# Kernel tuning notes

Hardware: AMD Instinct MI355X
Metric: run time of the kernel (lower is better)

The kernel has to match this reference:

```python
import jax, jax.numpy as jnp
import numpy as np

D_MODEL = 1024
NUM_HEAD = 16
D_HEAD = 64


def setup_inputs() -> dict:
    key = jax.random.key(0)
    ks = jax.random.split(key, 9)
    b, p = 8, 1024
    s = 1.0 / np.sqrt(D_MODEL)
    inp = {
        "x": jax.random.normal(ks[0], (b, p, D_MODEL), jnp.float32),
        "w_q": jax.random.uniform(ks[1], (D_MODEL, D_MODEL), jnp.float32, -s, s),
        "b_q": jax.random.uniform(ks[2], (D_MODEL,), jnp.float32, -s, s),
        "w_k": jax.random.uniform(ks[3], (D_MODEL, D_MODEL), jnp.float32, -s, s),
        "b_k": jax.random.uniform(ks[4], (D_MODEL,), jnp.float32, -s, s),
        "w_v": jax.random.uniform(ks[5], (D_MODEL, D_MODEL), jnp.float32, -s, s),
        "b_v": jax.random.uniform(ks[6], (D_MODEL,), jnp.float32, -s, s),
        "w_o": jax.random.uniform(ks[7], (D_MODEL, D_MODEL), jnp.float32, -s, s),
        "b_o": jax.random.uniform(ks[8], (D_MODEL,), jnp.float32, -s, s),
    }
    return inp


def reference(x, w_q, b_q, w_k, b_k, w_v, b_v, w_o, b_o):
    b, p, _ = x.shape
    # projections (torch Linear: y = x @ W.T + b; here weights stored [in,out])
    q = x @ w_q + b_q
    k = x @ w_k + b_k
    v = x @ w_v + b_v
    # [b, h, p, d]
    q = q.reshape(b, p, NUM_HEAD, D_HEAD).transpose(0, 2, 1, 3)
    k = k.reshape(b, p, NUM_HEAD, D_HEAD).transpose(0, 2, 1, 3)
    v = v.reshape(b, p, NUM_HEAD, D_HEAD).transpose(0, 2, 1, 3)
    scale = 1.0 / np.sqrt(D_HEAD).astype(np.float32)
    scores = jnp.einsum("bhqd,bhkd->bhqk", q, k) * scale
    attn = jax.nn.softmax(scores, axis=-1)
    out = jnp.einsum("bhqk,bhkd->bhqd", attn, v)
    out = out.transpose(0, 2, 1, 3).reshape(b, p, D_MODEL)
    return out @ w_o + b_o
```

## Files before the change

kernel.cpp:

```cpp
#include <hip/hip_runtime.h>
#include <stdint.h>


typedef __attribute__((ext_vector_type(8))) short short8;
typedef __attribute__((ext_vector_type(4))) short s16x4;
typedef __attribute__((ext_vector_type(4))) float f32x4;

__device__ __forceinline__ short f2bf(float f) {
  unsigned u = __builtin_bit_cast(unsigned, f);
  u += 0x7fffu + ((u >> 16) & 1u);
  return (short)(u >> 16);
}

__device__ __forceinline__ unsigned pk2bf(float a, float b) {
  unsigned ua = __builtin_bit_cast(unsigned, a);
  unsigned ub = __builtin_bit_cast(unsigned, b);
  ua += 0x7fffu + ((ua >> 16) & 1u);
  ub += 0x7fffu + ((ub >> 16) & 1u);
  return (ua >> 16) | (ub & 0xffff0000u);
}

typedef __attribute__((address_space(3))) void lds_void;
typedef __attribute__((address_space(1))) void gbl_void;
#define GLD16(gp, lp) \
  __builtin_amdgcn_global_load_lds((gbl_void*)(gp), (lds_void*)(lp), 16, 0, 0)

#define MFMA(a, b, c) __builtin_amdgcn_mfma_f32_16x16x32_bf16((a), (b), (c), 0, 0, 0)

__global__ __launch_bounds__(256) void k_convert(const float* __restrict__ src,
                                                 short* __restrict__ dst) {
  int i = (blockIdx.x * 256 + threadIdx.x) * 8;
  const float4* s = (const float4*)(src + i);
  float4 f0 = s[0], f1 = s[1];
  short8 o;
  o[0] = f2bf(f0.x); o[1] = f2bf(f0.y); o[2] = f2bf(f0.z); o[3] = f2bf(f0.w);
  o[4] = f2bf(f1.x); o[5] = f2bf(f1.y); o[6] = f2bf(f1.z); o[7] = f2bf(f1.w);
  *(short8*)(dst + i) = o;
}

__global__ __launch_bounds__(256) void k_transpose4(const float* __restrict__ s0,
                                                    const float* __restrict__ s1,
                                                    const float* __restrict__ s2,
                                                    const float* __restrict__ s3,
                                                    short* __restrict__ d0,
                                                    short* __restrict__ d1,
                                                    short* __restrict__ d2,
                                                    short* __restrict__ d3) {
  __shared__ float tile[32][33];
  const float* srcs[4] = {s0, s1, s2, s3};
  short* dsts[4] = {d0, d1, d2, d3};
  const float* src = srcs[blockIdx.z];
  short* dst = dsts[blockIdx.z];
  int tx = threadIdx.x, ty = threadIdx.y;
  int x0 = blockIdx.x * 32, y0 = blockIdx.y * 32;
#pragma unroll
  for (int i = 0; i < 32; i += 8)
    tile[ty + i][tx] = src[(y0 + ty + i) * 1024 + x0 + tx];
  __syncthreads();
#pragma unroll
  for (int i = 0; i < 32; i += 8)
    dst[(x0 + ty + i) * 1024 + y0 + tx] = f2bf(tile[tx][ty + i]);
}

template <int MODE>
__global__ __launch_bounds__(256, 3) void k_gemm(const short* __restrict__ A,
                                                 const short* __restrict__ Bt,
                                                 const float* __restrict__ bias0,
                                                 const float* __restrict__ bias1,
                                                 const float* __restrict__ bias2,
                                                 short* __restrict__ o0,
                                                 short* __restrict__ o1,
                                                 short* __restrict__ o2,
                                                 float* __restrict__ of) {
  __shared__ __align__(16) short a_lds[128 * 64];
  __shared__ __align__(16) short b_lds[128 * 64];
  const int tid = threadIdx.x;
  const int m0 = blockIdx.y * 128;
  const int n0 = blockIdx.x * 128;
  const int w = tid >> 6;
  const int lane = tid & 63;
  const int ll = lane & 15;
  const int qd = lane >> 4;
  const int wm = (w & 1) * 64;
  const int wn = (w >> 1) * 64;

  const int srow = tid >> 3;
  const int schunk = ((tid & 7) ^ (srow & 7)) * 8;
  const short* ag = A + (long)(m0 + srow) * 1024 + schunk;
  const short* bg = Bt + (long)(n0 + srow) * 1024 + schunk;

  f32x4 acc[4][4] = {};

  for (int kt = 0; kt < 1024; kt += 64) {
#pragma unroll
    for (int j = 0; j < 4; ++j) {
      GLD16(ag + j * 32768 + kt, &a_lds[j * 2048 + tid * 8]);
      GLD16(bg + j * 32768 + kt, &b_lds[j * 2048 + tid * 8]);
    }
    __syncthreads();
#pragma unroll
    for (int kh = 0; kh < 2; ++kh) {
      const int xoff = (((kh * 4 + qd) ^ (ll & 7)) * 8);
      short8 af[4], bfr[4];
#pragma unroll
      for (int mt = 0; mt < 4; ++mt)
        af[mt] = *(const short8*)&a_lds[(wm + mt * 16 + ll) * 64 + xoff];
#pragma unroll
      for (int nt = 0; nt < 4; ++nt)
        bfr[nt] = *(const short8*)&b_lds[(wn + nt * 16 + ll) * 64 + xoff];
#pragma unroll
      for (int mt = 0; mt < 4; ++mt)
#pragma unroll
        for (int nt = 0; nt < 4; ++nt)
          acc[mt][nt] = MFMA(af[mt], bfr[nt], acc[mt][nt]);
    }
    __syncthreads();
  }

  if (MODE == 0) {
#pragma unroll
    for (int nt = 0; nt < 4; ++nt) {
      int n = n0 + wn + nt * 16 + ll;
      int which = n >> 10;
      int nl = n & 1023;
      int h = nl >> 6, d = n & 63;
      if (which == 2) {
        float bv = bias2[nl];
        const int b = m0 >> 10;
        const int p0 = (m0 & 1023) + wm;
#pragma unroll
        for (int mt = 0; mt < 4; ++mt) {
          int p = p0 + mt * 16 + qd * 4;
          int2 pk;
          pk.x = (int)pk2bf(acc[mt][nt][0] + bv, acc[mt][nt][1] + bv);
          pk.y = (int)pk2bf(acc[mt][nt][2] + bv, acc[mt][nt][3] + bv);
          *(int2*)&o2[(long)(b * 16 + h) * 65536 + d * 1024 + p] = pk;
        }
      } else {
        float bv = (which == 0) ? bias0[nl] : bias1[nl];
        float sc = (which == 0) ? 0.125f : 1.0f;
        short* o = (which == 0) ? o0 : o1;
#pragma unroll
        for (int mt = 0; mt < 4; ++mt) {
#pragma unroll
          for (int r = 0; r < 4; ++r) {
            int m = m0 + wm + mt * 16 + qd * 4 + r;
            int b = m >> 10, p = m & 1023;
            o[(long)(b * 16 + h) * 65536 + p * 64 + d] = f2bf((acc[mt][nt][r] + bv) * sc);
          }
        }
      }
    }
  } else {
#pragma unroll
    for (int nt = 0; nt < 4; ++nt) {
      int n = n0 + wn + nt * 16 + ll;
      float bv = bias0[n];
#pragma unroll
      for (int mt = 0; mt < 4; ++mt) {
#pragma unroll
        for (int r = 0; r < 4; ++r) {
          int m = m0 + wm + mt * 16 + qd * 4 + r;
          of[(long)m * 1024 + n] = acc[mt][nt][r] + bv;
        }
      }
    }
  }
}

__global__ __launch_bounds__(256, 4) void k_attn(const short* __restrict__ Q,
                                                 const short* __restrict__ K,
                                                 const short* __restrict__ VT,
                                                 short* __restrict__ O) {
  __shared__ __align__(16) short k_lds[4096];
  __shared__ __align__(16) short vt_lds[4096];
  __shared__ __align__(16) short p_lds[4][32 * 72];
  const int tid = threadIdx.x;
  const int w = tid >> 6, lane = tid & 63, ll = lane & 15, qd = lane >> 4;
  const int bh = blockIdx.y, qb = blockIdx.x;
  const long hoff = (long)bh * 65536;
  const int qr0 = qb * 128 + w * 32;

  const short* qg = Q + hoff + (long)(qr0 + ll) * 64 + qd * 8;
  short8 qf[2][2];
  qf[0][0] = *(const short8*)qg;
  qf[0][1] = *(const short8*)(qg + 32);
  qf[1][0] = *(const short8*)(qg + 1024);
  qf[1][1] = *(const short8*)(qg + 1024 + 32);

  const int sr = tid >> 3;
  const int swz = (tid & 7) ^ (sr & 7);
  const short* kg = K + hoff + sr * 64 + swz * 8;
  const short* vg = VT + hoff + (long)sr * 1024 + swz * 8;
  short* kl0 = &k_lds[tid * 8];
  short* kl1 = &k_lds[2048 + tid * 8];
  short* vl0 = &vt_lds[tid * 8];
  short* vl1 = &vt_lds[2048 + tid * 8];

  const int swzr = ll & 7;
  const int fro0 = ll * 64 + ((qd ^ swzr) * 8);
  const int fro1 = ll * 64 + (((4 + qd) ^ swzr) * 8);
  short* pw = &p_lds[w][0];

  f32x4 oacc[2][4] = {};
  float l_part[2] = {0.f, 0.f};

  for (int c = 0; c < 16; ++c) {
    GLD16(kg + c * 4096, kl0);
    GLD16(kg + c * 4096 + 2048, kl1);
    GLD16(vg + c * 64, vl0);
    GLD16(vg + c * 64 + 32768, vl1);
    __syncthreads();

    f32x4 s[2][4];
#pragma unroll
    for (int jt = 0; jt < 4; ++jt) {
      short8 kf0 = *(const short8*)&k_lds[jt * 1024 + fro0];
      short8 kf1 = *(const short8*)&k_lds[jt * 1024 + fro1];
      f32x4 t0 = {};
      t0 = MFMA(kf0, qf[0][0], t0);
      t0 = MFMA(kf1, qf[0][1], t0);
      s[0][jt] = t0;
      f32x4 t1 = {};
      t1 = MFMA(kf0, qf[1][0], t1);
      t1 = MFMA(kf1, qf[1][1], t1);
      s[1][jt] = t1;
    }

    short8 pf[2][2];
#pragma unroll
    for (int g = 0; g < 2; ++g) {
      float rs = 0.f;
#pragma unroll
      for (int jt = 0; jt < 4; ++jt)
#pragma unroll
        for (int r = 0; r < 4; ++r) {
          float e = __expf(s[g][jt][r]);
          s[g][jt][r] = e;
          rs += e;
        }
      l_part[g] += rs;
      short* pg = pw + (g * 16 + ll) * 72;
#pragma unroll
      for (int jt = 0; jt < 4; ++jt) {
        int2 pk;
        pk.x = (int)pk2bf(s[g][jt][0], s[g][jt][1]);
        pk.y = (int)pk2bf(s[g][jt][2], s[g][jt][3]);
        *(int2*)&pg[jt * 16 + qd * 4] = pk;
      }
      pf[g][0] = *(const short8*)&pg[qd * 8];
      pf[g][1] = *(const short8*)&pg[32 + qd * 8];
    }

#pragma unroll
    for (int dt = 0; dt < 4; ++dt) {
      short8 vf0 = *(const short8*)&vt_lds[dt * 1024 + fro0];
      short8 vf1 = *(const short8*)&vt_lds[dt * 1024 + fro1];
      oacc[0][dt] = MFMA(vf0, pf[0][0], oacc[0][dt]);
      oacc[0][dt] = MFMA(vf1, pf[0][1], oacc[0][dt]);
      oacc[1][dt] = MFMA(vf0, pf[1][0], oacc[1][dt]);
      oacc[1][dt] = MFMA(vf1, pf[1][1], oacc[1][dt]);
    }
    __syncthreads();
  }

  const int b = bh >> 4, h = bh & 15;
#pragma unroll
  for (int g = 0; g < 2; ++g) {
    float l = l_part[g];
    l += __shfl_xor(l, 16, 64);
    l += __shfl_xor(l, 32, 64);
    const float inv = 1.0f / l;
    const long row = (long)(b * 1024 + qr0 + g * 16 + ll);
#pragma unroll
    for (int dt = 0; dt < 4; ++dt) {
      int2 ov;
      ov.x = (int)pk2bf(oacc[g][dt][0] * inv, oacc[g][dt][1] * inv);
      ov.y = (int)pk2bf(oacc[g][dt][2] * inv, oacc[g][dt][3] * inv);
      *(int2*)&O[row * 1024 + h * 64 + dt * 16 + qd * 4] = ov;
    }
  }
}

extern "C" void kernel_launch(void* const* d_in, const int* in_sizes, int n_in,
                              void* d_out, int out_size, void* d_ws, size_t ws_size,
                              hipStream_t stream) {
  const float* x   = (const float*)d_in[0];
  const float* w_q = (const float*)d_in[1];
  const float* b_q = (const float*)d_in[2];
  const float* w_k = (const float*)d_in[3];
  const float* b_k = (const float*)d_in[4];
  const float* w_v = (const float*)d_in[5];
  const float* b_v = (const float*)d_in[6];
  const float* w_o = (const float*)d_in[7];
  const float* b_o = (const float*)d_in[8];

  char* ws = (char*)d_ws;
  short* xb    = (short*)(ws);
  short* wqkvT = (short*)(ws + (16ull << 20));
  short* woT   = (short*)(ws + (22ull << 20));
  short* qw    = (short*)(ws + (24ull << 20));
  short* kw    = (short*)(ws + (40ull << 20));
  short* vw    = (short*)(ws + (56ull << 20));

  k_convert<<<4096, 256, 0, stream>>>(x, xb);
  k_transpose4<<<dim3(32, 32, 4), dim3(32, 8), 0, stream>>>(
      w_q, w_k, w_v, w_o, wqkvT, wqkvT + (1 << 20), wqkvT + (2 << 20), woT);

  k_gemm<0><<<dim3(24, 64), 256, 0, stream>>>(xb, wqkvT, b_q, b_k, b_v,
                                              qw, kw, vw, nullptr);

  k_attn<<<dim3(8, 128), 256, 0, stream>>>(qw, kw, vw, xb);

  k_gemm<1><<<dim3(8, 64), 256, 0, stream>>>(xb, woT, b_o, nullptr, nullptr,
                                             nullptr, nullptr, nullptr, (float*)d_out);
}
```

Before: 242.4 us.

## Merge input conversion with weight transpose and remap GEMM block order

The x-to-bf16 conversion is folded into the weight transpose kernel as an extra z-slice, which removes one kernel launch. The GEMM grid is flattened to 1D, and the block index is remapped so that m-tiles are spread (interleaved by 8) while n-tiles advance slowest. The goal is better L2/MALL reuse of the weight tiles across concurrently running blocks. This relies on M being exactly 64 tiles of 128 rows.

```diff
diff --git a/kernel.cpp b/kernel.cpp
--- a/kernel.cpp
+++ b/kernel.cpp
@@ -27,25 +27,31 @@
 
 #define MFMA(a, b, c) __builtin_amdgcn_mfma_f32_16x16x32_bf16((a), (b), (c), 0, 0, 0)
 
-__global__ __launch_bounds__(256) void k_convert(const float* __restrict__ src,
-                                                 short* __restrict__ dst) {
-  int i = (blockIdx.x * 256 + threadIdx.x) * 8;
-  const float4* s = (const float4*)(src + i);
-  float4 f0 = s[0], f1 = s[1];
-  short8 o;
-  o[0] = f2bf(f0.x); o[1] = f2bf(f0.y); o[2] = f2bf(f0.z); o[3] = f2bf(f0.w);
-  o[4] = f2bf(f1.x); o[5] = f2bf(f1.y); o[6] = f2bf(f1.z); o[7] = f2bf(f1.w);
-  *(short8*)(dst + i) = o;
-}
-
-__global__ __launch_bounds__(256) void k_transpose4(const float* __restrict__ s0,
-                                                    const float* __restrict__ s1,
-                                                    const float* __restrict__ s2,
-                                                    const float* __restrict__ s3,
-                                                    short* __restrict__ d0,
-                                                    short* __restrict__ d1,
-                                                    short* __restrict__ d2,
-                                                    short* __restrict__ d3) {
+__global__ __launch_bounds__(256) void k_prep(const float* __restrict__ x,
+                                              short* __restrict__ xb,
+                                              const float* __restrict__ s0,
+                                              const float* __restrict__ s1,
+                                              const float* __restrict__ s2,
+                                              const float* __restrict__ s3,
+                                              short* __restrict__ d0,
+                                              short* __restrict__ d1,
+                                              short* __restrict__ d2,
+                                              short* __restrict__ d3) {
+  if (blockIdx.z == 4) {
+    int t = threadIdx.y * 32 + threadIdx.x;
+    int bid = blockIdx.y * 32 + blockIdx.x;
+#pragma unroll
+    for (int j = 0; j < 4; ++j) {
+      int i = (bid * 1024 + j * 256 + t) * 8;
+      const float4* s = (const float4*)(x + i);
+      float4 f0 = s[0], f1 = s[1];
+      short8 o;
+      o[0] = f2bf(f0.x); o[1] = f2bf(f0.y); o[2] = f2bf(f0.z); o[3] = f2bf(f0.w);
+      o[4] = f2bf(f1.x); o[5] = f2bf(f1.y); o[6] = f2bf(f1.z); o[7] = f2bf(f1.w);
+      *(short8*)(xb + i) = o;
+    }
+    return;
+  }
   __shared__ float tile[32][33];
   const float* srcs[4] = {s0, s1, s2, s3};
   short* dsts[4] = {d0, d1, d2, d3};
@@ -75,8 +81,9 @@
   __shared__ __align__(16) short a_lds[128 * 64];
   __shared__ __align__(16) short b_lds[128 * 64];
   const int tid = threadIdx.x;
-  const int m0 = blockIdx.y * 128;
-  const int n0 = blockIdx.x * 128;
+  const int l = blockIdx.x;
+  const int m0 = ((((l & 7) << 3) | ((l >> 3) & 7))) << 7;
+  const int n0 = (l >> 6) << 7;
   const int w = tid >> 6;
   const int lane = tid & 63;
   const int ll = lane & 15;
@@ -303,15 +310,15 @@
   short* kw    = (short*)(ws + (40ull << 20));
   short* vw    = (short*)(ws + (56ull << 20));
 
-  k_convert<<<4096, 256, 0, stream>>>(x, xb);
-  k_transpose4<<<dim3(32, 32, 4), dim3(32, 8), 0, stream>>>(
-      w_q, w_k, w_v, w_o, wqkvT, wqkvT + (1 << 20), wqkvT + (2 << 20), woT);
-
-  k_gemm<0><<<dim3(24, 64), 256, 0, stream>>>(xb, wqkvT, b_q, b_k, b_v,
-                                              qw, kw, vw, nullptr);
+  k_prep<<<dim3(32, 32, 5), dim3(32, 8), 0, stream>>>(
+      x, xb, w_q, w_k, w_v, w_o,
+      wqkvT, wqkvT + (1 << 20), wqkvT + (2 << 20), woT);
+
+  k_gemm<0><<<1536, 256, 0, stream>>>(xb, wqkvT, b_q, b_k, b_v,
+                                      qw, kw, vw, nullptr);
 
   k_attn<<<dim3(8, 128), 256, 0, stream>>>(qw, kw, vw, xb);
 
-  k_gemm<1><<<dim3(8, 64), 256, 0, stream>>>(xb, woT, b_o, nullptr, nullptr,
-                                             nullptr, nullptr, nullptr, (float*)d_out);
-}
+  k_gemm<1><<<512, 256, 0, stream>>>(xb, woT, b_o, nullptr, nullptr,
+                                     nullptr, nullptr, nullptr, (float*)d_out);
+}
```

Result: no change. 239.6 us (-1.2%).
